# Kernel optimization log

Measured on AMD Instinct MI355X. Metric: run time of the kernel, lower is better.

Reference implementation:

```python
import jax, jax.numpy as jnp
import numpy as np

N_FACES = 50000
C_IN = 256
C_OUT = 256
K = 9  # kernel_size ** 2
PAD_SIZE = N_FACES + 1


def _pad_features(x, face_is_pad):
    # Faithful to: padded_x = zeros(pad_size, C); padded_x[~face_is_pad] = x
    # rank[i] = position of row i among the non-pad slots (in order)
    rank = jnp.cumsum(~face_is_pad) - 1            # [P]
    rank = jnp.clip(rank, 0, x.shape[0] - 1)
    padded = jnp.where(face_is_pad[:, None], jnp.zeros((), x.dtype), x[rank])
    return padded                                   # [P, C_in]


def setup_inputs() -> dict:
    key = jax.random.key(0)
    k1, k2, k3 = jax.random.split(key, 3)
    x = jax.random.normal(k1, (N_FACES, C_IN), dtype=jnp.float32)
    weight = jax.random.normal(k2, (C_OUT, C_IN, 1, K), dtype=jnp.float32)
    bias = jnp.zeros((C_OUT,), dtype=jnp.float32)
    face_neighborhood = jax.random.randint(k3, (N_FACES, K), 0, PAD_SIZE, dtype=jnp.int64)
    # exactly one pad slot (the last one); sum(~face_is_pad) == N_FACES == x.shape[0]
    face_is_pad = jnp.zeros((PAD_SIZE,), dtype=bool).at[PAD_SIZE - 1].set(True)
    return {"x": x, "weight": weight, "bias": bias,
            "face_neighborhood": face_neighborhood,
            "face_is_pad": face_is_pad, "pad_size": PAD_SIZE}


def reference(x, weight, bias, face_neighborhood, face_is_pad, pad_size):
    # demodulation: per-output-channel L2 normalization of the weight
    dcoefs = jax.lax.rsqrt(jnp.sum(weight * weight, axis=(1, 2, 3)) + 1e-8)  # [O]
    w = weight * dcoefs[:, None, None, None]        # [O, I, 1, K]
    padded = _pad_features(x, face_is_pad)          # [P, I]
    gathered = padded[face_neighborhood]            # [N, K, I]
    # 1x9 conv over gathered neighbors == contraction over (I, K)
    out = jnp.einsum('nki,oik->no', gathered, w[:, :, 0, :]) + bias  # [N, O]
    return out
```

## Files before the change

### kernel.cpp

```cpp
#include <hip/hip_runtime.h>

#define NF    50000
#define PADP  50001
#define KN    9
#define KTOT  2304
#define NCHUNK 782
#define NT    72
#define BM    128
#define NBLK  391
#define TSZ   24576
#define RSZ   73728

#define WT_OFF   0u
#define FLAG_OFF 1179648u
#define CNT_OFF  1179904u
#define PADX_OFF 1183744u

typedef float f32x4 __attribute__((ext_vector_type(4)));
typedef __bf16 bf16x8 __attribute__((ext_vector_type(8)));

typedef const __attribute__((address_space(1))) unsigned int* gas_t;
typedef __attribute__((address_space(3))) unsigned int* las_t;

static __device__ __forceinline__ void gll16(const void* g, void* l) {
  __builtin_amdgcn_global_load_lds((gas_t)g, (las_t)l, 16, 0, 0);
}

static __device__ __forceinline__ unsigned short f2bf(float f) {
  unsigned int u = __builtin_bit_cast(unsigned int, f);
  u = u + 0x7fffu + ((u >> 16) & 1u);
  return (unsigned short)(u >> 16);
}


__global__ void k_prep(const float* __restrict__ w, unsigned short* __restrict__ wt,
                       const unsigned char* __restrict__ pad, int* __restrict__ cnt,
                       const unsigned int* __restrict__ raw, int* __restrict__ flag) {
  if (blockIdx.x < 256) {
    int o = blockIdx.x;
    int i = threadIdx.x;
    const float* wr = w + (o * 256 + i) * 9;
    float wv[9];
    float s = 0.f;
#pragma unroll
    for (int k = 0; k < 9; ++k) { wv[k] = wr[k]; s += wv[k] * wv[k]; }
#pragma unroll
    for (int d = 32; d >= 1; d >>= 1) s += __shfl_xor(s, d);
    __shared__ float red[4];
    if ((i & 63) == 0) red[i >> 6] = s;
    __syncthreads();
    float dc = rsqrtf(red[0] + red[1] + red[2] + red[3] + 1e-8f);
#pragma unroll
    for (int k = 0; k < 9; ++k)
      wt[o * KTOT + k * 256 + i] = f2bf(wv[k] * dc);
  } else {
    int cb = blockIdx.x - 256;
    int t = cb * 256 + threadIdx.x;
    bool ip = (t < PADP) ? (pad[t] != 0) : true;
    unsigned long long m = __ballot(ip);
    int c = t >> 6;
    if ((threadIdx.x & 63) == 0 && c < NCHUNK) cnt[c] = __popcll(m);
    if (cb == 0 && threadIdx.x < 64) {
      unsigned int v = raw[threadIdx.x * 2 + 1];
      unsigned long long nz = __ballot(v != 0u);
      if (threadIdx.x == 0) flag[0] = (nz == 0ull) ? 1 : 0;
    }
  }
}

__global__ __launch_bounds__(256) void k_rankpadx(
    const float* __restrict__ x, const unsigned char* __restrict__ pad,
    const int* __restrict__ cnt, unsigned short* __restrict__ padx) {
  const int c = blockIdx.x;
  const int tid = threadIdx.x, w = tid >> 6, lane = tid & 63;
  int s = 0;
  for (int i = tid; i < c; i += 256) s += cnt[i];
#pragma unroll
  for (int d = 32; d >= 1; d >>= 1) s += __shfl_xor(s, d);
  __shared__ int red[4];
  __shared__ int rnk[64];
  if (lane == 0) red[w] = s;
  __syncthreads();
  const int S = red[0] + red[1] + red[2] + red[3];
  if (w == 0) {
    int p = c * 64 + lane;
    bool ip = (p < PADP) ? (pad[p] != 0) : true;
    unsigned long long m = __ballot(ip);
    int before = __popcll(m & ((1ull << lane) - 1ull));
    rnk[lane] = ip ? -1 : (p - (S + before));
  }
  __syncthreads();
  const int col = lane * 4;
#pragma unroll
  for (int i = 0; i < 16; ++i) {
    int rl = i * 4 + w;
    int pp = c * 64 + rl;
    if (pp >= PADP) continue;
    int rr = rnk[rl];
    ushort4 ov;
    if (rr < 0) { ov.x = 0; ov.y = 0; ov.z = 0; ov.w = 0; }
    else {
      const float4 v = *(const float4*)(x + rr * 256 + col);
      ov.x = f2bf(v.x); ov.y = f2bf(v.y); ov.z = f2bf(v.z); ov.w = f2bf(v.w);
    }
    *(ushort4*)(padx + pp * 256 + col) = ov;
  }
}

__global__ __launch_bounds__(512, 2) void k_main(
    const unsigned short* __restrict__ padx,
    const unsigned short* __restrict__ wt,
    const void* __restrict__ nbr,
    const int* __restrict__ flag,
    const float* __restrict__ bias,
    float* __restrict__ out) {
  __shared__ __align__(16) unsigned char sm[78336];
  const int tid = threadIdx.x;
  const int wv = tid >> 6, lane = tid & 63;
  const int m0 = blockIdx.x * BM;
  int* idx_lds = (int*)(sm + RSZ);

  const int q = lane & 15, hi = lane >> 4;
  const int wm = wv >> 2, wn = wv & 3;

  float bv[4];
#pragma unroll
  for (int ni = 0; ni < 4; ++ni) bv[ni] = bias[wn * 64 + ni * 16 + q];

  const bool f64 = (flag[0] != 0);
  const long long* n64 = (const long long*)nbr;
  const int* n32 = (const int*)nbr;
  for (int e = tid; e < BM * 9; e += 512) {
    int f = m0 + e / 9;
    if (f >= NF) f = NF - 1;
    int k = e - (e / 9) * 9;
    idx_lds[e] = f64 ? (int)n64[f * KN + k] : n32[f * KN + k];
  }
  __syncthreads();

  const int rA = tid >> 2;
  const int srcsl = ((tid & 3) ^ ((tid >> 3) & 3)) * 8;
  const int aD  = tid * 16;
  const int bD0 = 8192 + tid * 16;
  const int bD1 = 16384 + tid * 16;
  const unsigned short* wtb0 = wt + rA * KTOT + srcsl;
  const unsigned short* wtb1 = wt + (128 + rA) * KTOT + srcsl;

  const int slotb = (hi ^ ((q >> 1) & 3)) * 16;
  int aoff[4], boff[4];
#pragma unroll
  for (int mi = 0; mi < 4; ++mi) aoff[mi] = (wm * 64 + mi * 16 + q) * 64 + slotb;
#pragma unroll
  for (int ni = 0; ni < 4; ++ni) boff[ni] = 8192 + (wn * 64 + ni * 16 + q) * 64 + slotb;

  f32x4 acc[4][4];
#pragma unroll
  for (int a = 0; a < 4; ++a)
#pragma unroll
    for (int b = 0; b < 4; ++b) {
      acc[a][b][0] = 0.f; acc[a][b][1] = 0.f; acc[a][b][2] = 0.f; acc[a][b][3] = 0.f;
    }

#define STAGE(u, slotbase) {                                  \
    const int c0_ = ((u) & 7) * 32;                           \
    const int gu_ = (u) >> 3;                                 \
    const int p_ = idx_lds[rA * 9 + gu_];                     \
    unsigned char* bb_ = sm + (slotbase);                     \
    const int kk_ = gu_ * 256 + c0_;                          \
    gll16(padx + p_ * 256 + c0_ + srcsl, bb_ + aD);           \
    gll16(wtb0 + kk_, bb_ + bD0);                             \
    gll16(wtb1 + kk_, bb_ + bD1); }

  STAGE(0, 0)
  STAGE(1, TSZ)

  int oW = 2 * TSZ;
  int oR = 0;
#pragma unroll 3
  for (int t = 0; t < NT; ++t) {
    __builtin_amdgcn_sched_barrier(0);
    {
      const int u = (t + 2 < NT) ? t + 2 : NT - 1;
      STAGE(u, oW)
    }
    __builtin_amdgcn_sched_barrier(0);
    asm volatile("s_waitcnt vmcnt(6)" ::: "memory");
    __builtin_amdgcn_s_barrier();
    __builtin_amdgcn_sched_barrier(0);
    {
      const unsigned char* rb = sm + oR;
      bf16x8 af[4], bf[4];
#pragma unroll
      for (int mi = 0; mi < 4; ++mi) af[mi] = *(const bf16x8*)(rb + aoff[mi]);
#pragma unroll
      for (int ni = 0; ni < 4; ++ni) bf[ni] = *(const bf16x8*)(rb + boff[ni]);
      __builtin_amdgcn_s_setprio(1);
#pragma unroll
      for (int mi = 0; mi < 4; ++mi)
#pragma unroll
        for (int ni = 0; ni < 4; ++ni)
          acc[mi][ni] = __builtin_amdgcn_mfma_f32_16x16x32_bf16(af[mi], bf[ni], acc[mi][ni], 0, 0, 0);
      __builtin_amdgcn_s_setprio(0);
    }
    __builtin_amdgcn_s_barrier();
    oW += TSZ; if (oW == RSZ) oW = 0;
    oR += TSZ; if (oR == RSZ) oR = 0;
  }
  asm volatile("s_waitcnt vmcnt(0)" ::: "memory");
#undef STAGE

#pragma unroll
  for (int ni = 0; ni < 4; ++ni) {
    const int col = wn * 64 + ni * 16 + q;
#pragma unroll
    for (int mi = 0; mi < 4; ++mi) {
#pragma unroll
      for (int rr = 0; rr < 4; ++rr) {
        const int row = m0 + wm * 64 + mi * 16 + hi * 4 + rr;
        if (row < NF) out[row * 256 + col] = acc[mi][ni][rr] + bv[ni];
      }
    }
  }
}

extern "C" void kernel_launch(void* const* d_in, const int* in_sizes, int n_in,
                              void* d_out, int out_size, void* d_ws, size_t ws_size,
                              hipStream_t stream) {
  const float* x = (const float*)d_in[0];
  const float* wfull = (const float*)d_in[1];
  const float* bias = (const float*)d_in[2];
  const void* nbr = d_in[3];
  const unsigned char* pad = (const unsigned char*)d_in[4];
  float* out = (float*)d_out;
  char* ws = (char*)d_ws;

  unsigned short* wt   = (unsigned short*)(ws + WT_OFF);
  int* flag            = (int*)(ws + FLAG_OFF);
  int* cnt             = (int*)(ws + CNT_OFF);
  unsigned short* padx = (unsigned short*)(ws + PADX_OFF);

  k_prep<<<452, 256, 0, stream>>>(wfull, wt, pad, cnt, (const unsigned int*)nbr, flag);
  k_rankpadx<<<NCHUNK, 256, 0, stream>>>(x, pad, cnt, padx);
  k_main<<<NBLK, 512, 0, stream>>>(padx, wt, nbr, flag, bias, out);
}
```

Measured before the change: 101.1 us.

## Split output columns across blocks and double-buffer register fragments with deeper prefetch

The main GEMM kernel now uses 256-thread blocks, each computing a 128x128 output tile, so there are twice as many blocks and two column halves per row block. The K loop is unrolled into groups of 8 with register double-buffering of the A/B fragments, so LDS reads for the next step overlap the MFMAs of the current one. It also keeps a three-deep LDS prefetch with one barrier per step and preloads neighbor indices. The aim is to hide load latency and raise occupancy to 3 blocks per CU. The cost is that each gathered A row is fetched twice, once per column half, and the schedule is more complex.

```diff
diff --git a/kernel.cpp b/kernel.cpp
--- a/kernel.cpp
+++ b/kernel.cpp
@@ -6,10 +6,9 @@
 #define KTOT  2304
 #define NCHUNK 782
 #define NT    72
-#define BM    128
-#define NBLK  391
-#define TSZ   24576
-#define RSZ   73728
+#define TSZ   16384
+#define RSZ   49152
+#define NBLK  782
 
 #define WT_OFF   0u
 #define FLAG_OFF 1179648u
@@ -107,30 +106,31 @@
   }
 }
 
-__global__ __launch_bounds__(512, 2) void k_main(
+__global__ __launch_bounds__(256, 3) void k_main(
     const unsigned short* __restrict__ padx,
     const unsigned short* __restrict__ wt,
     const void* __restrict__ nbr,
     const int* __restrict__ flag,
     const float* __restrict__ bias,
     float* __restrict__ out) {
-  __shared__ __align__(16) unsigned char sm[78336];
+  __shared__ __align__(16) unsigned char sm[53760];
   const int tid = threadIdx.x;
   const int wv = tid >> 6, lane = tid & 63;
-  const int m0 = blockIdx.x * BM;
+  const int mblk = blockIdx.x >> 1, nblk = blockIdx.x & 1;
+  const int m0 = mblk * 128, n0 = nblk * 128;
   int* idx_lds = (int*)(sm + RSZ);
 
   const int q = lane & 15, hi = lane >> 4;
-  const int wm = wv >> 2, wn = wv & 3;
+  const int wm = wv >> 1, wn = wv & 1;
 
   float bv[4];
 #pragma unroll
-  for (int ni = 0; ni < 4; ++ni) bv[ni] = bias[wn * 64 + ni * 16 + q];
+  for (int ni = 0; ni < 4; ++ni) bv[ni] = bias[n0 + wn * 64 + ni * 16 + q];
 
   const bool f64 = (flag[0] != 0);
   const long long* n64 = (const long long*)nbr;
   const int* n32 = (const int*)nbr;
-  for (int e = tid; e < BM * 9; e += 512) {
+  for (int e = tid; e < 128 * 9; e += 256) {
     int f = m0 + e / 9;
     if (f >= NF) f = NF - 1;
     int k = e - (e / 9) * 9;
@@ -140,11 +140,12 @@
 
   const int rA = tid >> 2;
   const int srcsl = ((tid & 3) ^ ((tid >> 3) & 3)) * 8;
-  const int aD  = tid * 16;
+  const int aD0 = tid * 16;
+  const int aD1 = 4096 + tid * 16;
   const int bD0 = 8192 + tid * 16;
-  const int bD1 = 16384 + tid * 16;
-  const unsigned short* wtb0 = wt + rA * KTOT + srcsl;
-  const unsigned short* wtb1 = wt + (128 + rA) * KTOT + srcsl;
+  const int bD1 = 12288 + tid * 16;
+  const unsigned short* wtb0 = wt + (n0 + rA) * KTOT + srcsl;
+  const unsigned short* wtb1 = wt + (n0 + 64 + rA) * KTOT + srcsl;
 
   const int slotb = (hi ^ ((q >> 1) & 3)) * 16;
   int aoff[4], boff[4];
@@ -161,57 +162,94 @@
       acc[a][b][0] = 0.f; acc[a][b][1] = 0.f; acc[a][b][2] = 0.f; acc[a][b][3] = 0.f;
     }
 
-#define STAGE(u, slotbase) {                                  \
-    const int c0_ = ((u) & 7) * 32;                           \
-    const int gu_ = (u) >> 3;                                 \
-    const int p_ = idx_lds[rA * 9 + gu_];                     \
-    unsigned char* bb_ = sm + (slotbase);                     \
-    const int kk_ = gu_ * 256 + c0_;                          \
-    gll16(padx + p_ * 256 + c0_ + srcsl, bb_ + aD);           \
-    gll16(wtb0 + kk_, bb_ + bD0);                             \
-    gll16(wtb1 + kk_, bb_ + bD1); }
-
-  STAGE(0, 0)
-  STAGE(1, TSZ)
-
-  int oW = 2 * TSZ;
-  int oR = 0;
-#pragma unroll 3
-  for (int t = 0; t < NT; ++t) {
-    __builtin_amdgcn_sched_barrier(0);
-    {
-      const int u = (t + 2 < NT) ? t + 2 : NT - 1;
-      STAGE(u, oW)
-    }
-    __builtin_amdgcn_sched_barrier(0);
-    asm volatile("s_waitcnt vmcnt(6)" ::: "memory");
-    __builtin_amdgcn_s_barrier();
-    __builtin_amdgcn_sched_barrier(0);
-    {
-      const unsigned char* rb = sm + oR;
-      bf16x8 af[4], bf[4];
-#pragma unroll
-      for (int mi = 0; mi < 4; ++mi) af[mi] = *(const bf16x8*)(rb + aoff[mi]);
-#pragma unroll
-      for (int ni = 0; ni < 4; ++ni) bf[ni] = *(const bf16x8*)(rb + boff[ni]);
-      __builtin_amdgcn_s_setprio(1);
-#pragma unroll
-      for (int mi = 0; mi < 4; ++mi)
-#pragma unroll
-        for (int ni = 0; ni < 4; ++ni)
-          acc[mi][ni] = __builtin_amdgcn_mfma_f32_16x16x32_bf16(af[mi], bf[ni], acc[mi][ni], 0, 0, 0);
-      __builtin_amdgcn_s_setprio(0);
-    }
-    __builtin_amdgcn_s_barrier();
-    oW += TSZ; if (oW == RSZ) oW = 0;
-    oR += TSZ; if (oR == RSZ) oR = 0;
-  }
+  int pc0 = idx_lds[rA * 9 + 0], pc1 = idx_lds[(64 + rA) * 9 + 0];
+  int pn0 = idx_lds[rA * 9 + 1], pn1 = idx_lds[(64 + rA) * 9 + 1];
+  int pq0 = pn0, pq1 = pn1;
+
+#pragma unroll
+  for (int u = 0; u < 3; ++u) {
+    unsigned char* wb = sm + u * TSZ;
+    gll16(padx + pc0 * 256 + u * 32 + srcsl, wb + aD0);
+    gll16(padx + pc1 * 256 + u * 32 + srcsl, wb + aD1);
+    gll16(wtb0 + u * 32, wb + bD0);
+    gll16(wtb1 + u * 32, wb + bD1);
+  }
+  asm volatile("s_waitcnt vmcnt(4)" ::: "memory");
+  __builtin_amdgcn_s_barrier();
+
+  bf16x8 af0[4], bf0[4], af1[4], bf1[4];
+#pragma unroll
+  for (int mi = 0; mi < 4; ++mi) af0[mi] = *(const bf16x8*)(sm + aoff[mi]);
+#pragma unroll
+  for (int ni = 0; ni < 4; ++ni) bf0[ni] = *(const bf16x8*)(sm + boff[ni]);
+  asm volatile("s_waitcnt lgkmcnt(0)" ::: "memory");
+  __builtin_amdgcn_sched_barrier(0);
+  __builtin_amdgcn_s_barrier();
+
+  int oR = TSZ;
+  int oW = 0;
+
+#define ITER(J, cA, cB, nA, nB) {                                          \
+  const unsigned char* rb_ = sm + oR;                                      \
+  _Pragma("unroll")                                                        \
+  for (int mi = 0; mi < 4; ++mi) nA[mi] = *(const bf16x8*)(rb_ + aoff[mi]);\
+  _Pragma("unroll")                                                        \
+  for (int ni = 0; ni < 4; ++ni) nB[ni] = *(const bf16x8*)(rb_ + boff[ni]);\
+  {                                                                        \
+    const int u_ = g8 + (J) + 3;                                           \
+    const bool real_ = (u_ < NT);                                          \
+    const int c0_ = real_ ? (((J) + 3) & 7) * 32 : 224;                    \
+    const int kg_ = (real_ ? u_ : NT - 1) * 32;                            \
+    const int pA0_ = ((J) >= 5 && real_) ? pn0 : pc0;                      \
+    const int pA1_ = ((J) >= 5 && real_) ? pn1 : pc1;                      \
+    unsigned char* wb_ = sm + oW;                                          \
+    gll16(padx + pA0_ * 256 + c0_ + srcsl, wb_ + aD0);                     \
+    gll16(padx + pA1_ * 256 + c0_ + srcsl, wb_ + aD1);                     \
+    gll16(wtb0 + kg_, wb_ + bD0);                                          \
+    gll16(wtb1 + kg_, wb_ + bD1);                                          \
+  }                                                                        \
+  if ((J) == 0) {                                                          \
+    const int gn_ = (g + 2 > 8) ? 8 : g + 2;                               \
+    pq0 = idx_lds[rA * 9 + gn_];                                           \
+    pq1 = idx_lds[(64 + rA) * 9 + gn_];                                    \
+  }                                                                        \
+  __builtin_amdgcn_sched_barrier(0);                                       \
+  __builtin_amdgcn_s_setprio(1);                                           \
+  _Pragma("unroll")                                                        \
+  for (int mi = 0; mi < 4; ++mi)                                           \
+    _Pragma("unroll")                                                      \
+    for (int ni = 0; ni < 4; ++ni)                                         \
+      acc[mi][ni] = __builtin_amdgcn_mfma_f32_16x16x32_bf16(               \
+          cA[mi], cB[ni], acc[mi][ni], 0, 0, 0);                           \
+  __builtin_amdgcn_s_setprio(0);                                           \
+  __builtin_amdgcn_sched_barrier(0);                                       \
+  asm volatile("s_waitcnt vmcnt(4)" ::: "memory");                         \
+  asm volatile("s_waitcnt lgkmcnt(0)" ::: "memory");                       \
+  __builtin_amdgcn_sched_barrier(0);                                       \
+  __builtin_amdgcn_s_barrier();                                            \
+  oR += TSZ; if (oR == RSZ) oR = 0;                                        \
+  oW += TSZ; if (oW == RSZ) oW = 0;                                        \
+}
+
+#pragma unroll 1
+  for (int g = 0; g < 9; ++g) {
+    const int g8 = g * 8;
+    ITER(0, af0, bf0, af1, bf1)
+    ITER(1, af1, bf1, af0, bf0)
+    ITER(2, af0, bf0, af1, bf1)
+    ITER(3, af1, bf1, af0, bf0)
+    ITER(4, af0, bf0, af1, bf1)
+    ITER(5, af1, bf1, af0, bf0)
+    ITER(6, af0, bf0, af1, bf1)
+    ITER(7, af1, bf1, af0, bf0)
+    pc0 = pn0; pc1 = pn1; pn0 = pq0; pn1 = pq1;
+  }
+#undef ITER
   asm volatile("s_waitcnt vmcnt(0)" ::: "memory");
-#undef STAGE
 
 #pragma unroll
   for (int ni = 0; ni < 4; ++ni) {
-    const int col = wn * 64 + ni * 16 + q;
+    const int col = n0 + wn * 64 + ni * 16 + q;
 #pragma unroll
     for (int mi = 0; mi < 4; ++mi) {
 #pragma unroll
@@ -241,5 +279,5 @@
 
   k_prep<<<452, 256, 0, stream>>>(wfull, wt, pad, cnt, (const unsigned int*)nbr, flag);
   k_rankpadx<<<NCHUNK, 256, 0, stream>>>(x, pad, cnt, padx);
-  k_main<<<NBLK, 512, 0, stream>>>(padx, wt, nbr, flag, bias, out);
-}
+  k_main<<<NBLK, 256, 0, stream>>>(padx, wt, nbr, flag, bias, out);
+}
```

Measured after the change: 123.5 us. 1.22x slower.

## Load gathered A fragments directly into registers, stage only weights through LDS

Applied to the files above, without the earlier changes.

The gathered neighbor feature rows (A operand) are now loaded from global memory straight into MFMA register fragments, double-buffered in registers, instead of going through LDS. Only the weight tiles stay in a three-slot LDS ring, so per-stage LDS shrinks and the neighbor-index table in LDS goes away; neighbor indices are read per lane and prefetched one group ahead. This removes LDS write/read traffic and the index-staging barrier. The cost is uncoalesced 16-byte register gathers that sit on the MFMA critical path, and more register pressure.

```diff
diff --git a/kernel.cpp b/kernel.cpp
--- a/kernel.cpp
+++ b/kernel.cpp
@@ -8,8 +8,8 @@
 #define NT    72
 #define BM    128
 #define NBLK  391
-#define TSZ   24576
-#define RSZ   73728
+#define SLOT  16384
+#define RSZ   49152
 
 #define WT_OFF   0u
 #define FLAG_OFF 1179648u
@@ -114,44 +114,39 @@
     const int* __restrict__ flag,
     const float* __restrict__ bias,
     float* __restrict__ out) {
-  __shared__ __align__(16) unsigned char sm[78336];
+  __shared__ __align__(16) unsigned char sm[RSZ];
   const int tid = threadIdx.x;
   const int wv = tid >> 6, lane = tid & 63;
   const int m0 = blockIdx.x * BM;
-  int* idx_lds = (int*)(sm + RSZ);
-
   const int q = lane & 15, hi = lane >> 4;
   const int wm = wv >> 2, wn = wv & 3;
+  const int hi8 = hi * 8;
 
   float bv[4];
 #pragma unroll
   for (int ni = 0; ni < 4; ++ni) bv[ni] = bias[wn * 64 + ni * 16 + q];
 
   const bool f64 = (flag[0] != 0);
-  const long long* n64 = (const long long*)nbr;
-  const int* n32 = (const int*)nbr;
-  for (int e = tid; e < BM * 9; e += 512) {
-    int f = m0 + e / 9;
-    if (f >= NF) f = NF - 1;
-    int k = e - (e / 9) * 9;
-    idx_lds[e] = f64 ? (int)n64[f * KN + k] : n32[f * KN + k];
-  }
-  __syncthreads();
-
-  const int rA = tid >> 2;
+  const char* nb = (const char*)nbr;
+  int fb0, fb1, fb2, fb3;
+  {
+    int f0 = m0 + wm * 64 + 0 * 16 + q; if (f0 > NF - 1) f0 = NF - 1;
+    int f1 = m0 + wm * 64 + 1 * 16 + q; if (f1 > NF - 1) f1 = NF - 1;
+    int f2 = m0 + wm * 64 + 2 * 16 + q; if (f2 > NF - 1) f2 = NF - 1;
+    int f3 = m0 + wm * 64 + 3 * 16 + q; if (f3 > NF - 1) f3 = NF - 1;
+    fb0 = f0 * 9; fb1 = f1 * 9; fb2 = f2 * 9; fb3 = f3 * 9;
+  }
+#define LDIDX(fb, gg) (f64 ? (int)*(const long long*)(nb + ((fb) + (gg)) * 8) \
+                           : *(const int*)(nb + ((fb) + (gg)) * 4))
+
   const int srcsl = ((tid & 3) ^ ((tid >> 3) & 3)) * 8;
-  const int aD  = tid * 16;
-  const int bD0 = 8192 + tid * 16;
-  const int bD1 = 16384 + tid * 16;
-  const unsigned short* wtb0 = wt + rA * KTOT + srcsl;
-  const unsigned short* wtb1 = wt + (128 + rA) * KTOT + srcsl;
+  const unsigned short* wtb0 = wt + (tid >> 2) * KTOT + srcsl;
+  const unsigned short* wtb1 = wt + (128 + (tid >> 2)) * KTOT + srcsl;
 
   const int slotb = (hi ^ ((q >> 1) & 3)) * 16;
-  int aoff[4], boff[4];
-#pragma unroll
-  for (int mi = 0; mi < 4; ++mi) aoff[mi] = (wm * 64 + mi * 16 + q) * 64 + slotb;
-#pragma unroll
-  for (int ni = 0; ni < 4; ++ni) boff[ni] = 8192 + (wn * 64 + ni * 16 + q) * 64 + slotb;
+  int boff[4];
+#pragma unroll
+  for (int ni = 0; ni < 4; ++ni) boff[ni] = (wn * 64 + ni * 16 + q) * 64 + slotb;
 
   f32x4 acc[4][4];
 #pragma unroll
@@ -161,53 +156,101 @@
       acc[a][b][0] = 0.f; acc[a][b][1] = 0.f; acc[a][b][2] = 0.f; acc[a][b][3] = 0.f;
     }
 
-#define STAGE(u, slotbase) {                                  \
-    const int c0_ = ((u) & 7) * 32;                           \
-    const int gu_ = (u) >> 3;                                 \
-    const int p_ = idx_lds[rA * 9 + gu_];                     \
-    unsigned char* bb_ = sm + (slotbase);                     \
-    const int kk_ = gu_ * 256 + c0_;                          \
-    gll16(padx + p_ * 256 + c0_ + srcsl, bb_ + aD);           \
-    gll16(wtb0 + kk_, bb_ + bD0);                             \
-    gll16(wtb1 + kk_, bb_ + bD1); }
-
-  STAGE(0, 0)
-  STAGE(1, TSZ)
-
-  int oW = 2 * TSZ;
-  int oR = 0;
-#pragma unroll 3
-  for (int t = 0; t < NT; ++t) {
-    __builtin_amdgcn_sched_barrier(0);
-    {
-      const int u = (t + 2 < NT) ? t + 2 : NT - 1;
-      STAGE(u, oW)
-    }
-    __builtin_amdgcn_sched_barrier(0);
-    asm volatile("s_waitcnt vmcnt(6)" ::: "memory");
-    __builtin_amdgcn_s_barrier();
-    __builtin_amdgcn_sched_barrier(0);
-    {
-      const unsigned char* rb = sm + oR;
-      bf16x8 af[4], bf[4];
-#pragma unroll
-      for (int mi = 0; mi < 4; ++mi) af[mi] = *(const bf16x8*)(rb + aoff[mi]);
-#pragma unroll
-      for (int ni = 0; ni < 4; ++ni) bf[ni] = *(const bf16x8*)(rb + boff[ni]);
-      __builtin_amdgcn_s_setprio(1);
-#pragma unroll
-      for (int mi = 0; mi < 4; ++mi)
-#pragma unroll
-        for (int ni = 0; ni < 4; ++ni)
-          acc[mi][ni] = __builtin_amdgcn_mfma_f32_16x16x32_bf16(af[mi], bf[ni], acc[mi][ni], 0, 0, 0);
-      __builtin_amdgcn_s_setprio(0);
-    }
-    __builtin_amdgcn_s_barrier();
-    oW += TSZ; if (oW == RSZ) oW = 0;
-    oR += TSZ; if (oR == RSZ) oR = 0;
-  }
+  int rc0 = LDIDX(fb0, 0), rc1 = LDIDX(fb1, 0), rc2 = LDIDX(fb2, 0), rc3 = LDIDX(fb3, 0);
+  int rn0 = rc0, rn1 = rc1, rn2 = rc2, rn3 = rc3;
+  gll16(wtb0 + 0,  sm + 0 + tid * 16);
+  gll16(wtb1 + 0,  sm + 8192 + tid * 16);
+  gll16(wtb0 + 32, sm + SLOT + tid * 16);
+  gll16(wtb1 + 32, sm + SLOT + 8192 + tid * 16);
+  bf16x8 a0_0, a0_1, a0_2, a0_3, a1_0, a1_1, a1_2, a1_3;
+  a0_0 = *(const bf16x8*)(padx + rc0 * 256 + hi8);
+  a0_1 = *(const bf16x8*)(padx + rc1 * 256 + hi8);
+  a0_2 = *(const bf16x8*)(padx + rc2 * 256 + hi8);
+  a0_3 = *(const bf16x8*)(padx + rc3 * 256 + hi8);
+  asm volatile("s_waitcnt vmcnt(4)" ::: "memory");
+  __builtin_amdgcn_s_barrier();
+  bf16x8 b0_0, b0_1, b0_2, b0_3, b1_0, b1_1, b1_2, b1_3;
+  b0_0 = *(const bf16x8*)(sm + boff[0]);
+  b0_1 = *(const bf16x8*)(sm + boff[1]);
+  b0_2 = *(const bf16x8*)(sm + boff[2]);
+  b0_3 = *(const bf16x8*)(sm + boff[3]);
+
+  int oR = SLOT;
+  int oW = 2 * SLOT;
+
+#define MFMA16(cA0,cA1,cA2,cA3, cB0,cB1,cB2,cB3) {                          \
+    acc[0][0] = __builtin_amdgcn_mfma_f32_16x16x32_bf16(cA0, cB0, acc[0][0], 0,0,0); \
+    acc[0][1] = __builtin_amdgcn_mfma_f32_16x16x32_bf16(cA0, cB1, acc[0][1], 0,0,0); \
+    acc[0][2] = __builtin_amdgcn_mfma_f32_16x16x32_bf16(cA0, cB2, acc[0][2], 0,0,0); \
+    acc[0][3] = __builtin_amdgcn_mfma_f32_16x16x32_bf16(cA0, cB3, acc[0][3], 0,0,0); \
+    acc[1][0] = __builtin_amdgcn_mfma_f32_16x16x32_bf16(cA1, cB0, acc[1][0], 0,0,0); \
+    acc[1][1] = __builtin_amdgcn_mfma_f32_16x16x32_bf16(cA1, cB1, acc[1][1], 0,0,0); \
+    acc[1][2] = __builtin_amdgcn_mfma_f32_16x16x32_bf16(cA1, cB2, acc[1][2], 0,0,0); \
+    acc[1][3] = __builtin_amdgcn_mfma_f32_16x16x32_bf16(cA1, cB3, acc[1][3], 0,0,0); \
+    acc[2][0] = __builtin_amdgcn_mfma_f32_16x16x32_bf16(cA2, cB0, acc[2][0], 0,0,0); \
+    acc[2][1] = __builtin_amdgcn_mfma_f32_16x16x32_bf16(cA2, cB1, acc[2][1], 0,0,0); \
+    acc[2][2] = __builtin_amdgcn_mfma_f32_16x16x32_bf16(cA2, cB2, acc[2][2], 0,0,0); \
+    acc[2][3] = __builtin_amdgcn_mfma_f32_16x16x32_bf16(cA2, cB3, acc[2][3], 0,0,0); \
+    acc[3][0] = __builtin_amdgcn_mfma_f32_16x16x32_bf16(cA3, cB0, acc[3][0], 0,0,0); \
+    acc[3][1] = __builtin_amdgcn_mfma_f32_16x16x32_bf16(cA3, cB1, acc[3][1], 0,0,0); \
+    acc[3][2] = __builtin_amdgcn_mfma_f32_16x16x32_bf16(cA3, cB2, acc[3][2], 0,0,0); \
+    acc[3][3] = __builtin_amdgcn_mfma_f32_16x16x32_bf16(cA3, cB3, acc[3][3], 0,0,0); }
+
+#define ITER(J, cA0,cA1,cA2,cA3, cB0,cB1,cB2,cB3, nA0,nA1,nA2,nA3, nB0,nB1,nB2,nB3, R0,R1,R2,R3) { \
+    const unsigned char* rb_ = sm + oR;                                     \
+    nB0 = *(const bf16x8*)(rb_ + boff[0]);                                  \
+    nB1 = *(const bf16x8*)(rb_ + boff[1]);                                  \
+    nB2 = *(const bf16x8*)(rb_ + boff[2]);                                  \
+    nB3 = *(const bf16x8*)(rb_ + boff[3]);                                  \
+    if ((J) == 0) {                                                         \
+      const int gn_ = (g >= 8) ? 8 : g + 1;                                 \
+      rn0 = LDIDX(fb0, gn_); rn1 = LDIDX(fb1, gn_);                         \
+      rn2 = LDIDX(fb2, gn_); rn3 = LDIDX(fb3, gn_);                         \
+    }                                                                       \
+    {                                                                       \
+      const int kt2_ = g8 + (J) + 2;                                        \
+      const int kg_ = ((kt2_ < NT) ? kt2_ : NT - 1) * 32;                   \
+      gll16(wtb0 + kg_, sm + oW + tid * 16);                                \
+      gll16(wtb1 + kg_, sm + oW + 8192 + tid * 16);                         \
+    }                                                                       \
+    __builtin_amdgcn_sched_barrier(0);                                      \
+    {                                                                       \
+      const int kc_ = (((J) + 1) & 7) * 32 + hi8;                           \
+      nA0 = *(const bf16x8*)(padx + (R0) * 256 + kc_);                      \
+      nA1 = *(const bf16x8*)(padx + (R1) * 256 + kc_);                      \
+      nA2 = *(const bf16x8*)(padx + (R2) * 256 + kc_);                      \
+      nA3 = *(const bf16x8*)(padx + (R3) * 256 + kc_);                      \
+    }                                                                       \
+    __builtin_amdgcn_sched_barrier(0);                                      \
+    __builtin_amdgcn_s_setprio(1);                                          \
+    MFMA16(cA0,cA1,cA2,cA3, cB0,cB1,cB2,cB3)                                \
+    __builtin_amdgcn_s_setprio(0);                                          \
+    __builtin_amdgcn_sched_barrier(0);                                      \
+    asm volatile("s_waitcnt vmcnt(4)" ::: "memory");                        \
+    asm volatile("s_waitcnt lgkmcnt(0)" ::: "memory");                      \
+    __builtin_amdgcn_sched_barrier(0);                                      \
+    __builtin_amdgcn_s_barrier();                                           \
+    oR += SLOT; if (oR == RSZ) oR = 0;                                      \
+    oW += SLOT; if (oW == RSZ) oW = 0;                                      \
+  }
+
+#pragma unroll 1
+  for (int g = 0; g < 9; ++g) {
+    const int g8 = g * 8;
+    ITER(0, a0_0,a0_1,a0_2,a0_3, b0_0,b0_1,b0_2,b0_3, a1_0,a1_1,a1_2,a1_3, b1_0,b1_1,b1_2,b1_3, rc0,rc1,rc2,rc3)
+    ITER(1, a1_0,a1_1,a1_2,a1_3, b1_0,b1_1,b1_2,b1_3, a0_0,a0_1,a0_2,a0_3, b0_0,b0_1,b0_2,b0_3, rc0,rc1,rc2,rc3)
+    ITER(2, a0_0,a0_1,a0_2,a0_3, b0_0,b0_1,b0_2,b0_3, a1_0,a1_1,a1_2,a1_3, b1_0,b1_1,b1_2,b1_3, rc0,rc1,rc2,rc3)
+    ITER(3, a1_0,a1_1,a1_2,a1_3, b1_0,b1_1,b1_2,b1_3, a0_0,a0_1,a0_2,a0_3, b0_0,b0_1,b0_2,b0_3, rc0,rc1,rc2,rc3)
+    ITER(4, a0_0,a0_1,a0_2,a0_3, b0_0,b0_1,b0_2,b0_3, a1_0,a1_1,a1_2,a1_3, b1_0,b1_1,b1_2,b1_3, rc0,rc1,rc2,rc3)
+    ITER(5, a1_0,a1_1,a1_2,a1_3, b1_0,b1_1,b1_2,b1_3, a0_0,a0_1,a0_2,a0_3, b0_0,b0_1,b0_2,b0_3, rc0,rc1,rc2,rc3)
+    ITER(6, a0_0,a0_1,a0_2,a0_3, b0_0,b0_1,b0_2,b0_3, a1_0,a1_1,a1_2,a1_3, b1_0,b1_1,b1_2,b1_3, rc0,rc1,rc2,rc3)
+    ITER(7, a1_0,a1_1,a1_2,a1_3, b1_0,b1_1,b1_2,b1_3, a0_0,a0_1,a0_2,a0_3, b0_0,b0_1,b0_2,b0_3, rn0,rn1,rn2,rn3)
+    rc0 = rn0; rc1 = rn1; rc2 = rn2; rc3 = rn3;
+  }
+#undef ITER
+#undef MFMA16
+#undef LDIDX
   asm volatile("s_waitcnt vmcnt(0)" ::: "memory");
-#undef STAGE
 
 #pragma unroll
   for (int ni = 0; ni < 4; ++ni) {
```

Result: slower. 215.6 us (+113.3%).

## Load weight fragments directly to registers and shrink LDS to double buffer

Applied to the files above, without the earlier changes.

The main GEMM kernel no longer stages weight tiles through LDS. Each wave now reads its B fragments straight from global memory into registers, ping-ponging between two register sets. Only the gathered A rows still go through LDS, now double-buffered instead of triple-buffered, which cuts shared memory from about 78KB to 21KB and raises the launch-bounds occupancy hint to 4 blocks per CU. This trades LDS traffic and footprint for redundant global and L2 weight reads across waves, a shallower prefetch, and a full __syncthreads each iteration.

```diff
diff --git a/kernel.cpp b/kernel.cpp
--- a/kernel.cpp
+++ b/kernel.cpp
@@ -8,8 +8,6 @@
 #define NT    72
 #define BM    128
 #define NBLK  391
-#define TSZ   24576
-#define RSZ   73728
 
 #define WT_OFF   0u
 #define FLAG_OFF 1179648u
@@ -107,18 +105,18 @@
   }
 }
 
-__global__ __launch_bounds__(512, 2) void k_main(
+__global__ __launch_bounds__(512, 4) void k_main(
     const unsigned short* __restrict__ padx,
     const unsigned short* __restrict__ wt,
     const void* __restrict__ nbr,
     const int* __restrict__ flag,
     const float* __restrict__ bias,
     float* __restrict__ out) {
-  __shared__ __align__(16) unsigned char sm[78336];
+  __shared__ __align__(16) unsigned char sm[20992];
   const int tid = threadIdx.x;
   const int wv = tid >> 6, lane = tid & 63;
   const int m0 = blockIdx.x * BM;
-  int* idx_lds = (int*)(sm + RSZ);
+  int* idx_lds = (int*)(sm + 16384);
 
   const int q = lane & 15, hi = lane >> 4;
   const int wm = wv >> 2, wn = wv & 3;
@@ -140,18 +138,17 @@
 
   const int rA = tid >> 2;
   const int srcsl = ((tid & 3) ^ ((tid >> 3) & 3)) * 8;
-  const int aD  = tid * 16;
-  const int bD0 = 8192 + tid * 16;
-  const int bD1 = 16384 + tid * 16;
-  const unsigned short* wtb0 = wt + rA * KTOT + srcsl;
-  const unsigned short* wtb1 = wt + (128 + rA) * KTOT + srcsl;
+  const int aDst = tid * 16;
 
   const int slotb = (hi ^ ((q >> 1) & 3)) * 16;
-  int aoff[4], boff[4];
+  int aoff[4];
 #pragma unroll
   for (int mi = 0; mi < 4; ++mi) aoff[mi] = (wm * 64 + mi * 16 + q) * 64 + slotb;
-#pragma unroll
-  for (int ni = 0; ni < 4; ++ni) boff[ni] = 8192 + (wn * 64 + ni * 16 + q) * 64 + slotb;
+
+  const unsigned short* wB0 = wt + (wn * 64 +  0 + q) * KTOT + hi * 8;
+  const unsigned short* wB1 = wt + (wn * 64 + 16 + q) * KTOT + hi * 8;
+  const unsigned short* wB2 = wt + (wn * 64 + 32 + q) * KTOT + hi * 8;
+  const unsigned short* wB3 = wt + (wn * 64 + 48 + q) * KTOT + hi * 8;
 
   f32x4 acc[4][4];
 #pragma unroll
@@ -161,53 +158,49 @@
       acc[a][b][0] = 0.f; acc[a][b][1] = 0.f; acc[a][b][2] = 0.f; acc[a][b][3] = 0.f;
     }
 
-#define STAGE(u, slotbase) {                                  \
-    const int c0_ = ((u) & 7) * 32;                           \
-    const int gu_ = (u) >> 3;                                 \
-    const int p_ = idx_lds[rA * 9 + gu_];                     \
-    unsigned char* bb_ = sm + (slotbase);                     \
-    const int kk_ = gu_ * 256 + c0_;                          \
-    gll16(padx + p_ * 256 + c0_ + srcsl, bb_ + aD);           \
-    gll16(wtb0 + kk_, bb_ + bD0);                             \
-    gll16(wtb1 + kk_, bb_ + bD1); }
-
-  STAGE(0, 0)
-  STAGE(1, TSZ)
-
-  int oW = 2 * TSZ;
-  int oR = 0;
-#pragma unroll 3
-  for (int t = 0; t < NT; ++t) {
-    __builtin_amdgcn_sched_barrier(0);
-    {
-      const int u = (t + 2 < NT) ? t + 2 : NT - 1;
-      STAGE(u, oW)
-    }
-    __builtin_amdgcn_sched_barrier(0);
-    asm volatile("s_waitcnt vmcnt(6)" ::: "memory");
-    __builtin_amdgcn_s_barrier();
-    __builtin_amdgcn_sched_barrier(0);
-    {
-      const unsigned char* rb = sm + oR;
-      bf16x8 af[4], bf[4];
-#pragma unroll
-      for (int mi = 0; mi < 4; ++mi) af[mi] = *(const bf16x8*)(rb + aoff[mi]);
-#pragma unroll
-      for (int ni = 0; ni < 4; ++ni) bf[ni] = *(const bf16x8*)(rb + boff[ni]);
-      __builtin_amdgcn_s_setprio(1);
-#pragma unroll
-      for (int mi = 0; mi < 4; ++mi)
-#pragma unroll
-        for (int ni = 0; ni < 4; ++ni)
-          acc[mi][ni] = __builtin_amdgcn_mfma_f32_16x16x32_bf16(af[mi], bf[ni], acc[mi][ni], 0, 0, 0);
-      __builtin_amdgcn_s_setprio(0);
-    }
-    __builtin_amdgcn_s_barrier();
-    oW += TSZ; if (oW == RSZ) oW = 0;
-    oR += TSZ; if (oR == RSZ) oR = 0;
-  }
-  asm volatile("s_waitcnt vmcnt(0)" ::: "memory");
-#undef STAGE
+  {
+    const int p0 = idx_lds[rA * 9];
+    gll16(padx + p0 * 256 + srcsl, sm + aDst);
+  }
+  bf16x8 b00 = *(const bf16x8*)(wB0);
+  bf16x8 b01 = *(const bf16x8*)(wB1);
+  bf16x8 b02 = *(const bf16x8*)(wB2);
+  bf16x8 b03 = *(const bf16x8*)(wB3);
+  __syncthreads();
+  bf16x8 b10 = b00, b11 = b01, b12 = b02, b13 = b03;
+
+#define BITER(T, cB0,cB1,cB2,cB3, nB0,nB1,nB2,nB3) {                        \
+    const int u_ = (T) + 1;                                                 \
+    if (u_ < NT) {                                                          \
+      const int p_ = idx_lds[rA * 9 + (u_ >> 3)];                           \
+      gll16(padx + p_ * 256 + (u_ & 7) * 32 + srcsl,                        \
+            sm + (u_ & 1) * 8192 + aDst);                                   \
+      nB0 = *(const bf16x8*)(wB0 + u_ * 32);                                \
+      nB1 = *(const bf16x8*)(wB1 + u_ * 32);                                \
+      nB2 = *(const bf16x8*)(wB2 + u_ * 32);                                \
+      nB3 = *(const bf16x8*)(wB3 + u_ * 32);                                \
+    }                                                                       \
+    __builtin_amdgcn_sched_barrier(0);                                      \
+    {                                                                       \
+      const unsigned char* rb_ = sm + ((T) & 1) * 8192;                     \
+      _Pragma("unroll")                                                     \
+      for (int mi = 0; mi < 4; ++mi) {                                      \
+        bf16x8 af_ = *(const bf16x8*)(rb_ + aoff[mi]);                      \
+        acc[mi][0] = __builtin_amdgcn_mfma_f32_16x16x32_bf16(af_, cB0, acc[mi][0], 0,0,0); \
+        acc[mi][1] = __builtin_amdgcn_mfma_f32_16x16x32_bf16(af_, cB1, acc[mi][1], 0,0,0); \
+        acc[mi][2] = __builtin_amdgcn_mfma_f32_16x16x32_bf16(af_, cB2, acc[mi][2], 0,0,0); \
+        acc[mi][3] = __builtin_amdgcn_mfma_f32_16x16x32_bf16(af_, cB3, acc[mi][3], 0,0,0); \
+      }                                                                     \
+    }                                                                       \
+    __syncthreads();                                                        \
+  }
+
+#pragma unroll 1
+  for (int t2 = 0; t2 < NT; t2 += 2) {
+    BITER(t2,     b00,b01,b02,b03, b10,b11,b12,b13)
+    BITER(t2 + 1, b10,b11,b12,b13, b00,b01,b02,b03)
+  }
+#undef BITER
 
 #pragma unroll
   for (int ni = 0; ni < 4; ++ni) {
```

Result: slower. 186.4 us (+84.4%).
